# Optimization experiments

Hardware: AMD Instinct MI355X
Metric: run time of the kernel (lower is better)

Reference implementation:

```python
import jax, jax.numpy as jnp
import numpy as np


def _lstm(x, W, U, b, return_sequences):
    # x: [B,T,F]; W: [F,4H]; U: [H,4H]; b: [4H]. Keras gate order: i,f,c,o.
    B = x.shape[0]
    H = U.shape[0]
    # precompute input projection for all timesteps: [T,B,4H]
    xW = jnp.einsum('btf,fg->tbg', x, W) + b
    h0 = jnp.zeros((B, H), x.dtype)
    c0 = jnp.zeros((B, H), x.dtype)

    def step(carry, xw):
        h, c = carry
        z = xw + h @ U  # [B,4H]
        i, f, g, o = jnp.split(z, 4, axis=-1)
        i = jax.nn.sigmoid(i)
        f = jax.nn.sigmoid(f)
        g = jax.nn.relu(g)      # activation='relu' on candidate
        o = jax.nn.sigmoid(o)
        c = f * c + i * g
        h = o * jax.nn.relu(c)  # activation='relu' on cell output
        return (h, c), h

    (hT, _), hs = jax.lax.scan(step, (h0, c0), xW)
    if return_sequences:
        return jnp.transpose(hs, (1, 0, 2))  # [B,T,H]
    return hT  # [B,H]


def setup_inputs() -> dict:
    key = jax.random.key(0)
    ks = jax.random.split(key, 11)
    B, T, F = 512, 512, 64
    H1, H2, D1, D2 = 128, 64, 25, 1
    s = 0.05  # small weight scale keeps the relu-LSTM recurrence numerically stable
    return {
        'x':   jax.random.normal(ks[0], (B, T, F), jnp.float32),
        'W1':  jax.random.normal(ks[1], (F, 4 * H1), jnp.float32) * s,
        'U1':  jax.random.normal(ks[2], (H1, 4 * H1), jnp.float32) * s,
        'b1':  jnp.zeros((4 * H1,), jnp.float32),
        'W2':  jax.random.normal(ks[3], (H1, 4 * H2), jnp.float32) * s,
        'U2':  jax.random.normal(ks[4], (H2, 4 * H2), jnp.float32) * s,
        'b2':  jnp.zeros((4 * H2,), jnp.float32),
        'Wd1': jax.random.normal(ks[5], (H2, D1), jnp.float32) * s,
        'bd1': jnp.zeros((D1,), jnp.float32),
        'Wd2': jax.random.normal(ks[6], (D1, D2), jnp.float32) * s,
        'bd2': jnp.zeros((D2,), jnp.float32),
    }


def reference(x, W1, U1, b1, W2, U2, b2, Wd1, bd1, Wd2, bd2):
    h = _lstm(x, W1, U1, b1, return_sequences=True)   # [B,T,128]
    h = _lstm(h, W2, U2, b2, return_sequences=False)  # [B,64]
    h = h @ Wd1 + bd1                                  # [B,25]
    return h @ Wd2 + bd2                               # [B,1]
```

## Files before the change

kernel.cpp:

```cpp
#include <hip/hip_runtime.h>
#include <type_traits>

typedef _Float16 f16;
typedef _Float16 f16x4 __attribute__((ext_vector_type(4)));
typedef _Float16 f16x8 __attribute__((ext_vector_type(8)));
typedef float    f32x4 __attribute__((ext_vector_type(4)));

constexpr int TT = 512;
constexpr int FF = 64;
constexpr int H1 = 128;
constexpr int H2 = 64;
constexpr int D1 = 25;
constexpr int S1 = 136;
constexpr int S2 = 72;
constexpr int XC = 8;
constexpr float L2E = 1.44269504088896f;

__device__ __forceinline__ float sigm2(float z) {
    return __builtin_amdgcn_rcpf(1.f + __builtin_amdgcn_exp2f(-z));
}

__device__ __forceinline__ f32x4 mfma16(f16x8 a, f16x8 b, f32x4 c) {
    return __builtin_amdgcn_mfma_f32_16x16x32_f16(a, b, c, 0, 0, 0);
}

__device__ __forceinline__ void gl_lds16(const f16* g, f16* l) {
    __builtin_amdgcn_global_load_lds(
        (const __attribute__((address_space(1))) unsigned int*)g,
        (__attribute__((address_space(3))) unsigned int*)l, 16, 0, 0);
}

__global__ void cvt_x_kernel(const float* __restrict__ x, f16* __restrict__ xh) {
    const size_t i = ((size_t)blockIdx.x * blockDim.x + threadIdx.x) * 4;
    const float4 v = *(const float4*)(x + i);
    f16x4 h; h[0] = (f16)v.x; h[1] = (f16)v.y; h[2] = (f16)v.z; h[3] = (f16)v.w;
    *(f16x4*)(xh + i) = h;
}

__global__ __launch_bounds__(768, 3)
void lstm_pipe12(const f16* __restrict__ xh, const float* __restrict__ W1,
                 const float* __restrict__ U1, const float* __restrict__ b1,
                 const float* __restrict__ W2, const float* __restrict__ U2,
                 const float* __restrict__ b2, const float* __restrict__ Wd1,
                 const float* __restrict__ bd1,const float* __restrict__ Wd2,
                 const float* __restrict__ bd2, float* __restrict__ out)
{
    const int tid  = threadIdx.x;
    const int w    = tid >> 6;
    const int lane = tid & 63;
    const int quad = lane >> 4;
    const int lid  = lane & 15;
    const int b0   = blockIdx.x * 16;
    const bool isL1 = (w < 8);
    const int  j    = isL1 ? w : (w - 8);

    __shared__ __align__(16) f16 h1b[2][16][S1];
    __shared__ __align__(16) f16 h2b[2][16][S2];
    __shared__ __align__(16) f16 xlds[2][XC * 8 * 16 * 8];
    __shared__ float h2f[16][H2];
    __shared__ float dsh[16][D1];

    for (int i = tid; i < 2 * 16 * S1 / 2; i += 768) ((unsigned*)h1b)[i] = 0u;
    for (int i = tid; i < 2 * 16 * S2 / 2; i += 768) ((unsigned*)h2b)[i] = 0u;

    for (int s = tid; s < XC * 8 * 16; s += 768) {
        const int tl = s >> 7, fs = (s >> 4) & 7, row = s & 15;
        const f16* gp = xh + ((size_t)(b0 + row) * TT + tl) * FF + fs * 8;
        gl_lds16(gp, &xlds[0][(s >> 6) * 512]);
    }

    f16x8 wt[4][6];
    f32x4 bsp[4];
    float cs[4] = {0.f, 0.f, 0.f, 0.f};

    if (isL1) {
#pragma unroll
        for (int g = 0; g < 4; ++g) {
            const float sc = (g == 2) ? 1.f : L2E;
            const int n = 128 * g + 16 * w + lid;
#pragma unroll
            for (int rr = 0; rr < 4; ++rr)
                bsp[g][rr] = b1[128 * g + 16 * w + quad * 4 + rr] * sc;
#pragma unroll
            for (int c = 0; c < 4; ++c) {
                f16x8 f;
#pragma unroll
                for (int e = 0; e < 8; ++e)
                    f[e] = (f16)(U1[(32 * c + quad * 8 + e) * 512 + n] * sc);
                wt[g][c] = f;
            }
#pragma unroll
            for (int c = 0; c < 2; ++c) {
                f16x8 f;
#pragma unroll
                for (int e = 0; e < 8; ++e)
                    f[e] = (f16)(W1[(32 * c + quad * 8 + e) * 512 + n] * sc);
                wt[g][4 + c] = f;
            }
        }
    } else {
#pragma unroll
        for (int g = 0; g < 4; ++g) {
            const float sc = (g == 2) ? 1.f : L2E;
            const int n = 64 * g + 16 * j + lid;
#pragma unroll
            for (int rr = 0; rr < 4; ++rr)
                bsp[g][rr] = b2[64 * g + 16 * j + quad * 4 + rr] * sc;
#pragma unroll
            for (int c = 0; c < 4; ++c) {
                f16x8 f;
#pragma unroll
                for (int e = 0; e < 8; ++e)
                    f[e] = (f16)(W2[(32 * c + quad * 8 + e) * 256 + n] * sc);
                wt[g][c] = f;
            }
#pragma unroll
            for (int c = 0; c < 2; ++c) {
                f16x8 f;
#pragma unroll
                for (int e = 0; e < 8; ++e)
                    f[e] = (f16)(U2[(32 * c + quad * 8 + e) * 256 + n] * sc);
                wt[g][4 + c] = f;
            }
        }
    }
    __syncthreads();

    if (isL1) asm volatile("s_setprio 1");

    auto step = [&](auto parc, int i) {
        constexpr int PAR = decltype(parc)::value;
        constexpr int PR = PAR ^ 1;
        constexpr int PW = PAR;
        constexpr int QR = PAR;
        constexpr int QW = PAR ^ 1;
        if (isL1) {
            const f16* xc = &xlds[(i >> 3) & 1][(i & 7) * 1024];
            f16x8 fr0 = *(const f16x8*)&h1b[PR][lid][quad * 8];
            f16x8 fr1 = *(const f16x8*)&h1b[PR][lid][32 + quad * 8];
            f16x8 fr2 = *(const f16x8*)&h1b[PR][lid][64 + quad * 8];
            f16x8 fr3 = *(const f16x8*)&h1b[PR][lid][96 + quad * 8];
            f16x8 xf0 = *(const f16x8*)&xc[(quad * 16 + lid) * 8];
            f16x8 xf1 = *(const f16x8*)&xc[((4 + quad) * 16 + lid) * 8];
            f32x4 acc[4];
#pragma unroll
            for (int g = 0; g < 4; ++g) {
                f32x4 a = mfma16(wt[g][0], fr0, bsp[g]);
                a = mfma16(wt[g][1], fr1, a);
                a = mfma16(wt[g][2], fr2, a);
                a = mfma16(wt[g][3], fr3, a);
                a = mfma16(wt[g][4], xf0, a);
                a = mfma16(wt[g][5], xf1, a);
                acc[g] = a;
            }
            f16x4 hp;
#pragma unroll
            for (int r = 0; r < 4; ++r) {
                const float ig = sigm2(acc[0][r]);
                const float fg = sigm2(acc[1][r]);
                const float gg = fmaxf(acc[2][r], 0.f);
                const float og = sigm2(acc[3][r]);
                const float cc = fg * cs[r] + ig * gg;
                cs[r] = cc;
                hp[r] = (f16)(og * fmaxf(cc, 0.f));
            }
            *(f16x4*)&h1b[PW][lid][16 * w + quad * 4] = hp;
        } else {
            if (i >= 1) {
                f16x8 fr0 = *(const f16x8*)&h1b[PR][lid][quad * 8];
                f16x8 fr1 = *(const f16x8*)&h1b[PR][lid][32 + quad * 8];
                f16x8 fr2 = *(const f16x8*)&h1b[PR][lid][64 + quad * 8];
                f16x8 fr3 = *(const f16x8*)&h1b[PR][lid][96 + quad * 8];
                f16x8 fr4 = *(const f16x8*)&h2b[QR][lid][quad * 8];
                f16x8 fr5 = *(const f16x8*)&h2b[QR][lid][32 + quad * 8];
                f32x4 acc[4];
#pragma unroll
                for (int g = 0; g < 4; ++g) {
                    f32x4 a = mfma16(wt[g][0], fr0, bsp[g]);
                    a = mfma16(wt[g][1], fr1, a);
                    a = mfma16(wt[g][2], fr2, a);
                    a = mfma16(wt[g][3], fr3, a);
                    a = mfma16(wt[g][4], fr4, a);
                    a = mfma16(wt[g][5], fr5, a);
                    acc[g] = a;
                }
                f16x4 hp;
#pragma unroll
                for (int r = 0; r < 4; ++r) {
                    const float ig = sigm2(acc[0][r]);
                    const float fg = sigm2(acc[1][r]);
                    const float gg = fmaxf(acc[2][r], 0.f);
                    const float og = sigm2(acc[3][r]);
                    const float cc = fg * cs[r] + ig * gg;
                    cs[r] = cc;
                    hp[r] = (f16)(og * fmaxf(cc, 0.f));
                }
                *(f16x4*)&h2b[QW][lid][16 * j + quad * 4] = hp;
            }
        }
    };

    for (int ii = 0; ii < TT; ii += 2) {
        if ((ii & (XC - 1)) == 0 && ii + XC < TT) {
            const int nc = (ii >> 3) + 1;
            f16* dst = xlds[nc & 1];
            for (int s = tid; s < XC * 8 * 16; s += 768) {
                const int tl = s >> 7, fs = (s >> 4) & 7, row = s & 15;
                const f16* gp = xh + ((size_t)(b0 + row) * TT + (nc * XC + tl)) * FF + fs * 8;
                gl_lds16(gp, &dst[(s >> 6) * 512]);
            }
        }
        step(std::integral_constant<int, 0>{}, ii);
        __syncthreads();
        step(std::integral_constant<int, 1>{}, ii + 1);
        __syncthreads();
    }

    if (isL1) asm volatile("s_setprio 0");

    if (!isL1) {
        f16x8 fr0 = *(const f16x8*)&h1b[1][lid][quad * 8];
        f16x8 fr1 = *(const f16x8*)&h1b[1][lid][32 + quad * 8];
        f16x8 fr2 = *(const f16x8*)&h1b[1][lid][64 + quad * 8];
        f16x8 fr3 = *(const f16x8*)&h1b[1][lid][96 + quad * 8];
        f16x8 fr4 = *(const f16x8*)&h2b[0][lid][quad * 8];
        f16x8 fr5 = *(const f16x8*)&h2b[0][lid][32 + quad * 8];
        f32x4 acc[4];
#pragma unroll
        for (int g = 0; g < 4; ++g) {
            f32x4 a = mfma16(wt[g][0], fr0, bsp[g]);
            a = mfma16(wt[g][1], fr1, a);
            a = mfma16(wt[g][2], fr2, a);
            a = mfma16(wt[g][3], fr3, a);
            a = mfma16(wt[g][4], fr4, a);
            a = mfma16(wt[g][5], fr5, a);
            acc[g] = a;
        }
        float4 ho;
#pragma unroll
        for (int r = 0; r < 4; ++r) {
            const float ig = sigm2(acc[0][r]);
            const float fg = sigm2(acc[1][r]);
            const float gg = fmaxf(acc[2][r], 0.f);
            const float og = sigm2(acc[3][r]);
            const float cc = fg * cs[r] + ig * gg;
            (&ho.x)[r] = og * fmaxf(cc, 0.f);
        }
        *(float4*)&h2f[lid][16 * j + quad * 4] = ho;
    }
    __syncthreads();

    for (int idx = tid; idx < 16 * D1; idx += 768) {
        const int bq = idx / D1, p = idx % D1;
        float d = bd1[p];
#pragma unroll
        for (int k = 0; k < H2; ++k) d += h2f[bq][k] * Wd1[k * D1 + p];
        dsh[bq][p] = d * Wd2[p];
    }
    __syncthreads();
    if (tid < 16) {
        float o = bd2[0];
#pragma unroll
        for (int p = 0; p < D1; ++p) o += dsh[tid][p];
        out[b0 + tid] = o;
    }
}

extern "C" void kernel_launch(void* const* d_in, const int* in_sizes, int n_in,
                              void* d_out, int out_size, void* d_ws, size_t ws_size,
                              hipStream_t stream) {
    (void)in_sizes; (void)n_in; (void)out_size; (void)ws_size;
    const float* x   = (const float*)d_in[0];
    const float* W1  = (const float*)d_in[1];
    const float* U1  = (const float*)d_in[2];
    const float* b1  = (const float*)d_in[3];
    const float* W2  = (const float*)d_in[4];
    const float* U2  = (const float*)d_in[5];
    const float* b2  = (const float*)d_in[6];
    const float* Wd1 = (const float*)d_in[7];
    const float* bd1 = (const float*)d_in[8];
    const float* Wd2 = (const float*)d_in[9];
    const float* bd2 = (const float*)d_in[10];
    float* out = (float*)d_out;
    f16*   xh  = (f16*)d_ws;

    const int nx = 512 * 512 * 64;
    cvt_x_kernel<<<dim3(nx / (256 * 4)), dim3(256), 0, stream>>>(x, xh);
    lstm_pipe12<<<dim3(32), dim3(768), 0, stream>>>(
        xh, W1, U1, b1, W2, U2, b2, Wd1, bd1, Wd2, bd2, out);
}
```

Baseline: 680.7 us.

## Precompute layer-1 input projection in a parallel kernel before the recurrence

A new parallel kernel computes x@W1+b1 for all timesteps with MFMA and stores it as fp16 in the workspace (256 MB). The recurrent kernel then streams these precomputed gate inputs as the accumulator seed, so layer-1 waves drop the input-projection MFMAs from the serial critical path. In exchange it adds a large global write and read of the projected tensor and depends on workspace size, falling back to the old path otherwise.

```diff
diff --git a/kernel.cpp b/kernel.cpp
--- a/kernel.cpp
+++ b/kernel.cpp
@@ -29,6 +29,282 @@
         (const __attribute__((address_space(1))) unsigned int*)g,
         (__attribute__((address_space(3))) unsigned int*)l, 16, 0, 0);
 }
+
+
+__global__ __launch_bounds__(512)
+void prep_xw(const float* __restrict__ x, const float* __restrict__ W1,
+             const float* __restrict__ b1, f16* __restrict__ xw)
+{
+    __shared__ __align__(16) f16 wlds[512][72];
+    __shared__ __align__(16) float blds[512];
+    const int tid = threadIdx.x;
+
+    for (int idx = tid; idx < 64 * 512; idx += 512) {
+        const int k = idx >> 9, col = idx & 511;
+        const float sc = ((col >> 7) == 2) ? 1.f : L2E;
+        wlds[col][k] = (f16)(W1[idx] * sc);
+    }
+    blds[tid] = b1[tid] * (((tid >> 7) == 2) ? 1.f : L2E);
+    __syncthreads();
+
+    const int wv = tid >> 6, lane = tid & 63, quad = lane >> 4, lid = lane & 15;
+    const int row = blockIdx.x * 128 + wv * 16 + lid;
+
+    f16x8 xf[2];
+#pragma unroll
+    for (int c = 0; c < 2; ++c) {
+        const float4 v0 = *(const float4*)(x + (size_t)row * FF + 32 * c + quad * 8);
+        const float4 v1 = *(const float4*)(x + (size_t)row * FF + 32 * c + quad * 8 + 4);
+        f16x8 f;
+        f[0] = (f16)v0.x; f[1] = (f16)v0.y; f[2] = (f16)v0.z; f[3] = (f16)v0.w;
+        f[4] = (f16)v1.x; f[5] = (f16)v1.y; f[6] = (f16)v1.z; f[7] = (f16)v1.w;
+        xf[c] = f;
+    }
+
+#pragma unroll 4
+    for (int cg = 0; cg < 32; ++cg) {
+        const f16* wp = &wlds[16 * cg + lid][0];
+        const f16x8 a0 = *(const f16x8*)(wp + quad * 8);
+        const f16x8 a1 = *(const f16x8*)(wp + 32 + quad * 8);
+        const f32x4 bv = *(const f32x4*)&blds[16 * cg + quad * 4];
+        f32x4 acc = mfma16(a0, xf[0], bv);
+        acc = mfma16(a1, xf[1], acc);
+        f16x4 o;
+#pragma unroll
+        for (int r = 0; r < 4; ++r) o[r] = (f16)acc[r];
+        *(f16x4*)&xw[(size_t)row * 512 + 16 * cg + quad * 4] = o;
+    }
+}
+
+__global__ __launch_bounds__(768, 3)
+void lstm_pipe12_xw(const f16* __restrict__ xw, const float* __restrict__ U1,
+                    const float* __restrict__ W2, const float* __restrict__ U2,
+                    const float* __restrict__ b2, const float* __restrict__ Wd1,
+                    const float* __restrict__ bd1,const float* __restrict__ Wd2,
+                    const float* __restrict__ bd2, float* __restrict__ out)
+{
+    const int tid  = threadIdx.x;
+    const int w    = tid >> 6;
+    const int lane = tid & 63;
+    const int quad = lane >> 4;
+    const int lid  = lane & 15;
+    const int b0   = blockIdx.x * 16;
+    const bool isL1 = (w < 8);
+    const int  j    = isL1 ? w : (w - 8);
+
+    __shared__ __align__(16) f16 h1b[2][16][S1];
+    __shared__ __align__(16) f16 h2b[2][16][S2];
+    __shared__ float h2f[16][H2];
+    __shared__ float dsh[16][D1];
+
+    for (int i = tid; i < 2 * 16 * S1 / 2; i += 768) ((unsigned*)h1b)[i] = 0u;
+    for (int i = tid; i < 2 * 16 * S2 / 2; i += 768) ((unsigned*)h2b)[i] = 0u;
+
+    f16x8 wt[4][6];
+    f32x4 bsp[4];
+    float cs[4] = {0.f, 0.f, 0.f, 0.f};
+
+    if (isL1) {
+#pragma unroll
+        for (int g = 0; g < 4; ++g) {
+            const float sc = (g == 2) ? 1.f : L2E;
+            const int n = 128 * g + 16 * w + lid;
+#pragma unroll
+            for (int c = 0; c < 4; ++c) {
+                f16x8 f;
+#pragma unroll
+                for (int e = 0; e < 8; ++e)
+                    f[e] = (f16)(U1[(32 * c + quad * 8 + e) * 512 + n] * sc);
+                wt[g][c] = f;
+            }
+        }
+    } else {
+#pragma unroll
+        for (int g = 0; g < 4; ++g) {
+            const float sc = (g == 2) ? 1.f : L2E;
+            const int n = 64 * g + 16 * j + lid;
+#pragma unroll
+            for (int rr = 0; rr < 4; ++rr)
+                bsp[g][rr] = b2[64 * g + 16 * j + quad * 4 + rr] * sc;
+#pragma unroll
+            for (int c = 0; c < 4; ++c) {
+                f16x8 f;
+#pragma unroll
+                for (int e = 0; e < 8; ++e)
+                    f[e] = (f16)(W2[(32 * c + quad * 8 + e) * 256 + n] * sc);
+                wt[g][c] = f;
+            }
+#pragma unroll
+            for (int c = 0; c < 2; ++c) {
+                f16x8 f;
+#pragma unroll
+                for (int e = 0; e < 8; ++e)
+                    f[e] = (f16)(U2[(32 * c + quad * 8 + e) * 256 + n] * sc);
+                wt[g][4 + c] = f;
+            }
+        }
+    }
+
+    const f16* pxw = nullptr;
+    if (isL1) pxw = xw + (size_t)(b0 + lid) * TT * 512 + 16 * w + quad * 4;
+
+    f16x4 xa[2][4], xb[2][4];
+    if (isL1) {
+#pragma unroll
+        for (int g = 0; g < 4; ++g) {
+            xa[0][g] = *(const f16x4*)(pxw + (size_t)0 * 512 + 128 * g);
+            xa[1][g] = *(const f16x4*)(pxw + (size_t)1 * 512 + 128 * g);
+        }
+    }
+    __syncthreads();
+
+    if (isL1) asm volatile("s_setprio 1");
+
+    auto step = [&](auto parc, int i, const f16x4 (&xv)[4]) {
+        constexpr int PAR = decltype(parc)::value;
+        constexpr int PR = PAR ^ 1;
+        constexpr int PW = PAR;
+        constexpr int QR = PAR;
+        constexpr int QW = PAR ^ 1;
+        if (isL1) {
+            f16x8 fr0 = *(const f16x8*)&h1b[PR][lid][quad * 8];
+            f16x8 fr1 = *(const f16x8*)&h1b[PR][lid][32 + quad * 8];
+            f16x8 fr2 = *(const f16x8*)&h1b[PR][lid][64 + quad * 8];
+            f16x8 fr3 = *(const f16x8*)&h1b[PR][lid][96 + quad * 8];
+            f32x4 acc[4];
+#pragma unroll
+            for (int g = 0; g < 4; ++g) {
+                f32x4 ci;
+#pragma unroll
+                for (int r = 0; r < 4; ++r) ci[r] = (float)xv[g][r];
+                f32x4 a = mfma16(wt[g][0], fr0, ci);
+                a = mfma16(wt[g][1], fr1, a);
+                a = mfma16(wt[g][2], fr2, a);
+                a = mfma16(wt[g][3], fr3, a);
+                acc[g] = a;
+            }
+            f16x4 hp;
+#pragma unroll
+            for (int r = 0; r < 4; ++r) {
+                const float ig = sigm2(acc[0][r]);
+                const float fg = sigm2(acc[1][r]);
+                const float gg = fmaxf(acc[2][r], 0.f);
+                const float og = sigm2(acc[3][r]);
+                const float cc = fg * cs[r] + ig * gg;
+                cs[r] = cc;
+                hp[r] = (f16)(og * fmaxf(cc, 0.f));
+            }
+            *(f16x4*)&h1b[PW][lid][16 * w + quad * 4] = hp;
+        } else {
+            if (i >= 1) {
+                f16x8 fr0 = *(const f16x8*)&h1b[PR][lid][quad * 8];
+                f16x8 fr1 = *(const f16x8*)&h1b[PR][lid][32 + quad * 8];
+                f16x8 fr2 = *(const f16x8*)&h1b[PR][lid][64 + quad * 8];
+                f16x8 fr3 = *(const f16x8*)&h1b[PR][lid][96 + quad * 8];
+                f16x8 fr4 = *(const f16x8*)&h2b[QR][lid][quad * 8];
+                f16x8 fr5 = *(const f16x8*)&h2b[QR][lid][32 + quad * 8];
+                f32x4 acc[4];
+#pragma unroll
+                for (int g = 0; g < 4; ++g) {
+                    f32x4 a = mfma16(wt[g][0], fr0, bsp[g]);
+                    a = mfma16(wt[g][1], fr1, a);
+                    a = mfma16(wt[g][2], fr2, a);
+                    a = mfma16(wt[g][3], fr3, a);
+                    a = mfma16(wt[g][4], fr4, a);
+                    a = mfma16(wt[g][5], fr5, a);
+                    acc[g] = a;
+                }
+                f16x4 hp;
+#pragma unroll
+                for (int r = 0; r < 4; ++r) {
+                    const float ig = sigm2(acc[0][r]);
+                    const float fg = sigm2(acc[1][r]);
+                    const float gg = fmaxf(acc[2][r], 0.f);
+                    const float og = sigm2(acc[3][r]);
+                    const float cc = fg * cs[r] + ig * gg;
+                    cs[r] = cc;
+                    hp[r] = (f16)(og * fmaxf(cc, 0.f));
+                }
+                *(f16x4*)&h2b[QW][lid][16 * j + quad * 4] = hp;
+            }
+        }
+    };
+
+    for (int ii = 0; ii < TT; ii += 4) {
+        if (isL1) {
+#pragma unroll
+            for (int g = 0; g < 4; ++g) {
+                xb[0][g] = *(const f16x4*)(pxw + (size_t)(ii + 2) * 512 + 128 * g);
+                xb[1][g] = *(const f16x4*)(pxw + (size_t)(ii + 3) * 512 + 128 * g);
+            }
+        }
+        step(std::integral_constant<int, 0>{}, ii, xa[0]);
+        __syncthreads();
+        step(std::integral_constant<int, 1>{}, ii + 1, xa[1]);
+        __syncthreads();
+        if (isL1 && ii + 4 < TT) {
+#pragma unroll
+            for (int g = 0; g < 4; ++g) {
+                xa[0][g] = *(const f16x4*)(pxw + (size_t)(ii + 4) * 512 + 128 * g);
+                xa[1][g] = *(const f16x4*)(pxw + (size_t)(ii + 5) * 512 + 128 * g);
+            }
+        }
+        step(std::integral_constant<int, 0>{}, ii + 2, xb[0]);
+        __syncthreads();
+        step(std::integral_constant<int, 1>{}, ii + 3, xb[1]);
+        __syncthreads();
+    }
+
+    if (isL1) asm volatile("s_setprio 0");
+
+    if (!isL1) {
+        f16x8 fr0 = *(const f16x8*)&h1b[1][lid][quad * 8];
+        f16x8 fr1 = *(const f16x8*)&h1b[1][lid][32 + quad * 8];
+        f16x8 fr2 = *(const f16x8*)&h1b[1][lid][64 + quad * 8];
+        f16x8 fr3 = *(const f16x8*)&h1b[1][lid][96 + quad * 8];
+        f16x8 fr4 = *(const f16x8*)&h2b[0][lid][quad * 8];
+        f16x8 fr5 = *(const f16x8*)&h2b[0][lid][32 + quad * 8];
+        f32x4 acc[4];
+#pragma unroll
+        for (int g = 0; g < 4; ++g) {
+            f32x4 a = mfma16(wt[g][0], fr0, bsp[g]);
+            a = mfma16(wt[g][1], fr1, a);
+            a = mfma16(wt[g][2], fr2, a);
+            a = mfma16(wt[g][3], fr3, a);
+            a = mfma16(wt[g][4], fr4, a);
+            a = mfma16(wt[g][5], fr5, a);
+            acc[g] = a;
+        }
+        float4 ho;
+#pragma unroll
+        for (int r = 0; r < 4; ++r) {
+            const float ig = sigm2(acc[0][r]);
+            const float fg = sigm2(acc[1][r]);
+            const float gg = fmaxf(acc[2][r], 0.f);
+            const float og = sigm2(acc[3][r]);
+            const float cc = fg * cs[r] + ig * gg;
+            (&ho.x)[r] = og * fmaxf(cc, 0.f);
+        }
+        *(float4*)&h2f[lid][16 * j + quad * 4] = ho;
+    }
+    __syncthreads();
+
+    for (int idx = tid; idx < 16 * D1; idx += 768) {
+        const int bq = idx / D1, p = idx % D1;
+        float d = bd1[p];
+#pragma unroll
+        for (int k = 0; k < H2; ++k) d += h2f[bq][k] * Wd1[k * D1 + p];
+        dsh[bq][p] = d * Wd2[p];
+    }
+    __syncthreads();
+    if (tid < 16) {
+        float o = bd2[0];
+#pragma unroll
+        for (int p = 0; p < D1; ++p) o += dsh[tid][p];
+        out[b0 + tid] = o;
+    }
+}
+
 
 __global__ void cvt_x_kernel(const float* __restrict__ x, f16* __restrict__ xh) {
     const size_t i = ((size_t)blockIdx.x * blockDim.x + threadIdx.x) * 4;
@@ -269,7 +545,7 @@
 extern "C" void kernel_launch(void* const* d_in, const int* in_sizes, int n_in,
                               void* d_out, int out_size, void* d_ws, size_t ws_size,
                               hipStream_t stream) {
-    (void)in_sizes; (void)n_in; (void)out_size; (void)ws_size;
+    (void)in_sizes; (void)n_in; (void)out_size;
     const float* x   = (const float*)d_in[0];
     const float* W1  = (const float*)d_in[1];
     const float* U1  = (const float*)d_in[2];
@@ -282,10 +558,19 @@
     const float* Wd2 = (const float*)d_in[9];
     const float* bd2 = (const float*)d_in[10];
     float* out = (float*)d_out;
-    f16*   xh  = (f16*)d_ws;
-
-    const int nx = 512 * 512 * 64;
-    cvt_x_kernel<<<dim3(nx / (256 * 4)), dim3(256), 0, stream>>>(x, xh);
-    lstm_pipe12<<<dim3(32), dim3(768), 0, stream>>>(
-        xh, W1, U1, b1, W2, U2, b2, Wd1, bd1, Wd2, bd2, out);
-}
+
+    constexpr size_t XW_BYTES = (size_t)512 * 512 * 512 * sizeof(f16);
+
+    if (ws_size >= XW_BYTES) {
+        f16* xwp = (f16*)d_ws;
+        prep_xw<<<dim3(2048), dim3(512), 0, stream>>>(x, W1, b1, xwp);
+        lstm_pipe12_xw<<<dim3(32), dim3(768), 0, stream>>>(
+            xwp, U1, W2, U2, b2, Wd1, bd1, Wd2, bd2, out);
+    } else {
+        f16* xh = (f16*)d_ws;
+        const int nx = 512 * 512 * 64;
+        cvt_x_kernel<<<dim3(nx / (256 * 4)), dim3(256), 0, stream>>>(x, xh);
+        lstm_pipe12<<<dim3(32), dim3(768), 0, stream>>>(
+            xh, W1, U1, b1, W2, U2, b2, Wd1, bd1, Wd2, bd2, out);
+    }
+}
```

Result: slower. 1.483 ms (+117.9%).

## Consolidate LSTM layers into four waves each handling two L1 tiles and one L2 tile

Applied to the files above, without the earlier changes.

Shrinks the block from twelve waves (eight layer-1, four layer-2) to four waves, each computing two layer-1 gate column tiles and one layer-2 tile per step. The h and x fragments are loaded once per wave and reused across all three tiles, and the wave-priority hints are dropped. This aims to cut barrier cost and redundant LDS fragment loads, but triples the per-wave MFMA chain and register-resident weights, which risks longer serial latency and register spills.

```diff
diff --git a/kernel.cpp b/kernel.cpp
--- a/kernel.cpp
+++ b/kernel.cpp
@@ -37,13 +37,13 @@
     *(f16x4*)(xh + i) = h;
 }
 
-__global__ __launch_bounds__(768, 3)
-void lstm_pipe12(const f16* __restrict__ xh, const float* __restrict__ W1,
-                 const float* __restrict__ U1, const float* __restrict__ b1,
-                 const float* __restrict__ W2, const float* __restrict__ U2,
-                 const float* __restrict__ b2, const float* __restrict__ Wd1,
-                 const float* __restrict__ bd1,const float* __restrict__ Wd2,
-                 const float* __restrict__ bd2, float* __restrict__ out)
+__global__ __launch_bounds__(256, 1)
+void lstm_q4(const f16* __restrict__ xh, const float* __restrict__ W1,
+             const float* __restrict__ U1, const float* __restrict__ b1,
+             const float* __restrict__ W2, const float* __restrict__ U2,
+             const float* __restrict__ b2, const float* __restrict__ Wd1,
+             const float* __restrict__ bd1,const float* __restrict__ Wd2,
+             const float* __restrict__ bd2, float* __restrict__ out)
 {
     const int tid  = threadIdx.x;
     const int w    = tid >> 6;
@@ -51,8 +51,6 @@
     const int quad = lane >> 4;
     const int lid  = lane & 15;
     const int b0   = blockIdx.x * 16;
-    const bool isL1 = (w < 8);
-    const int  j    = isL1 ? w : (w - 8);
 
     __shared__ __align__(16) f16 h1b[2][16][S1];
     __shared__ __align__(16) f16 h2b[2][16][S2];
@@ -60,34 +58,37 @@
     __shared__ float h2f[16][H2];
     __shared__ float dsh[16][D1];
 
-    for (int i = tid; i < 2 * 16 * S1 / 2; i += 768) ((unsigned*)h1b)[i] = 0u;
-    for (int i = tid; i < 2 * 16 * S2 / 2; i += 768) ((unsigned*)h2b)[i] = 0u;
-
-    for (int s = tid; s < XC * 8 * 16; s += 768) {
+    for (int i = tid; i < 2 * 16 * S1 / 2; i += 256) ((unsigned*)h1b)[i] = 0u;
+    for (int i = tid; i < 2 * 16 * S2 / 2; i += 256) ((unsigned*)h2b)[i] = 0u;
+
+    for (int s = tid; s < XC * 8 * 16; s += 256) {
         const int tl = s >> 7, fs = (s >> 4) & 7, row = s & 15;
         const f16* gp = xh + ((size_t)(b0 + row) * TT + tl) * FF + fs * 8;
         gl_lds16(gp, &xlds[0][(s >> 6) * 512]);
     }
 
-    f16x8 wt[4][6];
-    f32x4 bsp[4];
-    float cs[4] = {0.f, 0.f, 0.f, 0.f};
-
-    if (isL1) {
+    f16x8 wtA[4][6], wtB[4][6], wtC[4][6];
+    f32x4 bspA[4], bspB[4], bspC[4];
+    float csA[4] = {0.f, 0.f, 0.f, 0.f};
+    float csB[4] = {0.f, 0.f, 0.f, 0.f};
+    float csC[4] = {0.f, 0.f, 0.f, 0.f};
+
+    {
+        const int cg = 2 * w;
 #pragma unroll
         for (int g = 0; g < 4; ++g) {
             const float sc = (g == 2) ? 1.f : L2E;
-            const int n = 128 * g + 16 * w + lid;
+            const int n = 128 * g + 16 * cg + lid;
 #pragma unroll
             for (int rr = 0; rr < 4; ++rr)
-                bsp[g][rr] = b1[128 * g + 16 * w + quad * 4 + rr] * sc;
+                bspA[g][rr] = b1[128 * g + 16 * cg + quad * 4 + rr] * sc;
 #pragma unroll
             for (int c = 0; c < 4; ++c) {
                 f16x8 f;
 #pragma unroll
                 for (int e = 0; e < 8; ++e)
                     f[e] = (f16)(U1[(32 * c + quad * 8 + e) * 512 + n] * sc);
-                wt[g][c] = f;
+                wtA[g][c] = f;
             }
 #pragma unroll
             for (int c = 0; c < 2; ++c) {
@@ -95,24 +96,52 @@
 #pragma unroll
                 for (int e = 0; e < 8; ++e)
                     f[e] = (f16)(W1[(32 * c + quad * 8 + e) * 512 + n] * sc);
-                wt[g][4 + c] = f;
-            }
-        }
-    } else {
+                wtA[g][4 + c] = f;
+            }
+        }
+    }
+    {
+        const int cg = 2 * w + 1;
 #pragma unroll
         for (int g = 0; g < 4; ++g) {
             const float sc = (g == 2) ? 1.f : L2E;
-            const int n = 64 * g + 16 * j + lid;
+            const int n = 128 * g + 16 * cg + lid;
 #pragma unroll
             for (int rr = 0; rr < 4; ++rr)
-                bsp[g][rr] = b2[64 * g + 16 * j + quad * 4 + rr] * sc;
+                bspB[g][rr] = b1[128 * g + 16 * cg + quad * 4 + rr] * sc;
 #pragma unroll
             for (int c = 0; c < 4; ++c) {
                 f16x8 f;
 #pragma unroll
                 for (int e = 0; e < 8; ++e)
+                    f[e] = (f16)(U1[(32 * c + quad * 8 + e) * 512 + n] * sc);
+                wtB[g][c] = f;
+            }
+#pragma unroll
+            for (int c = 0; c < 2; ++c) {
+                f16x8 f;
+#pragma unroll
+                for (int e = 0; e < 8; ++e)
+                    f[e] = (f16)(W1[(32 * c + quad * 8 + e) * 512 + n] * sc);
+                wtB[g][4 + c] = f;
+            }
+        }
+    }
+    {
+#pragma unroll
+        for (int g = 0; g < 4; ++g) {
+            const float sc = (g == 2) ? 1.f : L2E;
+            const int n = 64 * g + 16 * w + lid;
+#pragma unroll
+            for (int rr = 0; rr < 4; ++rr)
+                bspC[g][rr] = b2[64 * g + 16 * w + quad * 4 + rr] * sc;
+#pragma unroll
+            for (int c = 0; c < 4; ++c) {
+                f16x8 f;
+#pragma unroll
+                for (int e = 0; e < 8; ++e)
                     f[e] = (f16)(W2[(32 * c + quad * 8 + e) * 256 + n] * sc);
-                wt[g][c] = f;
+                wtC[g][c] = f;
             }
 #pragma unroll
             for (int c = 0; c < 2; ++c) {
@@ -120,13 +149,11 @@
 #pragma unroll
                 for (int e = 0; e < 8; ++e)
                     f[e] = (f16)(U2[(32 * c + quad * 8 + e) * 256 + n] * sc);
-                wt[g][4 + c] = f;
+                wtC[g][4 + c] = f;
             }
         }
     }
     __syncthreads();
-
-    if (isL1) asm volatile("s_setprio 1");
 
     auto step = [&](auto parc, int i) {
         constexpr int PAR = decltype(parc)::value;
@@ -134,69 +161,105 @@
         constexpr int PW = PAR;
         constexpr int QR = PAR;
         constexpr int QW = PAR ^ 1;
-        if (isL1) {
-            const f16* xc = &xlds[(i >> 3) & 1][(i & 7) * 1024];
-            f16x8 fr0 = *(const f16x8*)&h1b[PR][lid][quad * 8];
-            f16x8 fr1 = *(const f16x8*)&h1b[PR][lid][32 + quad * 8];
-            f16x8 fr2 = *(const f16x8*)&h1b[PR][lid][64 + quad * 8];
-            f16x8 fr3 = *(const f16x8*)&h1b[PR][lid][96 + quad * 8];
-            f16x8 xf0 = *(const f16x8*)&xc[(quad * 16 + lid) * 8];
-            f16x8 xf1 = *(const f16x8*)&xc[((4 + quad) * 16 + lid) * 8];
-            f32x4 acc[4];
+        const f16* xc = &xlds[(i >> 3) & 1][(i & 7) * 1024];
+        f16x8 xf0 = *(const f16x8*)&xc[(quad * 16 + lid) * 8];
+        f16x8 xf1 = *(const f16x8*)&xc[((4 + quad) * 16 + lid) * 8];
+        f16x8 fr0 = *(const f16x8*)&h1b[PR][lid][quad * 8];
+        f16x8 fr1 = *(const f16x8*)&h1b[PR][lid][32 + quad * 8];
+        f16x8 fr2 = *(const f16x8*)&h1b[PR][lid][64 + quad * 8];
+        f16x8 fr3 = *(const f16x8*)&h1b[PR][lid][96 + quad * 8];
+        f16x8 fr4 = *(const f16x8*)&h2b[QR][lid][quad * 8];
+        f16x8 fr5 = *(const f16x8*)&h2b[QR][lid][32 + quad * 8];
+
+        f32x4 accA[4];
+#pragma unroll
+        for (int g = 0; g < 4; ++g) {
+            f32x4 a = mfma16(wtA[g][0], fr0, bspA[g]);
+            a = mfma16(wtA[g][1], fr1, a);
+            a = mfma16(wtA[g][2], fr2, a);
+            a = mfma16(wtA[g][3], fr3, a);
+            a = mfma16(wtA[g][4], xf0, a);
+            a = mfma16(wtA[g][5], xf1, a);
+            accA[g] = a;
+        }
+        f32x4 accB[4];
+#pragma unroll
+        for (int g = 0; g < 4; ++g) {
+            f32x4 a = mfma16(wtB[g][0], fr0, bspB[g]);
+            a = mfma16(wtB[g][1], fr1, a);
+            a = mfma16(wtB[g][2], fr2, a);
+            a = mfma16(wtB[g][3], fr3, a);
+            a = mfma16(wtB[g][4], xf0, a);
+            a = mfma16(wtB[g][5], xf1, a);
+            accB[g] = a;
+        }
+        {
+            f16x4 hp;
+#pragma unroll
+            for (int r = 0; r < 4; ++r) {
+                const float ig = sigm2(accA[0][r]);
+                const float fg = sigm2(accA[1][r]);
+                const float gg = fmaxf(accA[2][r], 0.f);
+                const float og = sigm2(accA[3][r]);
+                const float cc = fg * csA[r] + ig * gg;
+                csA[r] = cc;
+                hp[r] = (f16)(og * fmaxf(cc, 0.f));
+            }
+            *(f16x4*)&h1b[PW][lid][16 * (2 * w) + quad * 4] = hp;
+        }
+        if (i >= 1) {
+            f32x4 accC[4];
 #pragma unroll
             for (int g = 0; g < 4; ++g) {
-                f32x4 a = mfma16(wt[g][0], fr0, bsp[g]);
-                a = mfma16(wt[g][1], fr1, a);
-                a = mfma16(wt[g][2], fr2, a);
-                a = mfma16(wt[g][3], fr3, a);
-                a = mfma16(wt[g][4], xf0, a);
-                a = mfma16(wt[g][5], xf1, a);
-                acc[g] = a;
-            }
-            f16x4 hp;
-#pragma unroll
-            for (int r = 0; r < 4; ++r) {
-                const float ig = sigm2(acc[0][r]);
-                const float fg = sigm2(acc[1][r]);
-                const float gg = fmaxf(acc[2][r], 0.f);
-                const float og = sigm2(acc[3][r]);
-                const float cc = fg * cs[r] + ig * gg;
-                cs[r] = cc;
-                hp[r] = (f16)(og * fmaxf(cc, 0.f));
-            }
-            *(f16x4*)&h1b[PW][lid][16 * w + quad * 4] = hp;
-        } else {
-            if (i >= 1) {
-                f16x8 fr0 = *(const f16x8*)&h1b[PR][lid][quad * 8];
-                f16x8 fr1 = *(const f16x8*)&h1b[PR][lid][32 + quad * 8];
-                f16x8 fr2 = *(const f16x8*)&h1b[PR][lid][64 + quad * 8];
-                f16x8 fr3 = *(const f16x8*)&h1b[PR][lid][96 + quad * 8];
-                f16x8 fr4 = *(const f16x8*)&h2b[QR][lid][quad * 8];
-                f16x8 fr5 = *(const f16x8*)&h2b[QR][lid][32 + quad * 8];
-                f32x4 acc[4];
-#pragma unroll
-                for (int g = 0; g < 4; ++g) {
-                    f32x4 a = mfma16(wt[g][0], fr0, bsp[g]);
-                    a = mfma16(wt[g][1], fr1, a);
-                    a = mfma16(wt[g][2], fr2, a);
-                    a = mfma16(wt[g][3], fr3, a);
-                    a = mfma16(wt[g][4], fr4, a);
-                    a = mfma16(wt[g][5], fr5, a);
-                    acc[g] = a;
-                }
+                f32x4 a = mfma16(wtC[g][0], fr0, bspC[g]);
+                a = mfma16(wtC[g][1], fr1, a);
+                a = mfma16(wtC[g][2], fr2, a);
+                a = mfma16(wtC[g][3], fr3, a);
+                a = mfma16(wtC[g][4], fr4, a);
+                a = mfma16(wtC[g][5], fr5, a);
+                accC[g] = a;
+            }
+            {
                 f16x4 hp;
 #pragma unroll
                 for (int r = 0; r < 4; ++r) {
-                    const float ig = sigm2(acc[0][r]);
-                    const float fg = sigm2(acc[1][r]);
-                    const float gg = fmaxf(acc[2][r], 0.f);
-                    const float og = sigm2(acc[3][r]);
-                    const float cc = fg * cs[r] + ig * gg;
-                    cs[r] = cc;
+                    const float ig = sigm2(accB[0][r]);
+                    const float fg = sigm2(accB[1][r]);
+                    const float gg = fmaxf(accB[2][r], 0.f);
+                    const float og = sigm2(accB[3][r]);
+                    const float cc = fg * csB[r] + ig * gg;
+                    csB[r] = cc;
                     hp[r] = (f16)(og * fmaxf(cc, 0.f));
                 }
-                *(f16x4*)&h2b[QW][lid][16 * j + quad * 4] = hp;
-            }
+                *(f16x4*)&h1b[PW][lid][16 * (2 * w + 1) + quad * 4] = hp;
+            }
+            {
+                f16x4 hp;
+#pragma unroll
+                for (int r = 0; r < 4; ++r) {
+                    const float ig = sigm2(accC[0][r]);
+                    const float fg = sigm2(accC[1][r]);
+                    const float gg = fmaxf(accC[2][r], 0.f);
+                    const float og = sigm2(accC[3][r]);
+                    const float cc = fg * csC[r] + ig * gg;
+                    csC[r] = cc;
+                    hp[r] = (f16)(og * fmaxf(cc, 0.f));
+                }
+                *(f16x4*)&h2b[QW][lid][16 * w + quad * 4] = hp;
+            }
+        } else {
+            f16x4 hp;
+#pragma unroll
+            for (int r = 0; r < 4; ++r) {
+                const float ig = sigm2(accB[0][r]);
+                const float fg = sigm2(accB[1][r]);
+                const float gg = fmaxf(accB[2][r], 0.f);
+                const float og = sigm2(accB[3][r]);
+                const float cc = fg * csB[r] + ig * gg;
+                csB[r] = cc;
+                hp[r] = (f16)(og * fmaxf(cc, 0.f));
+            }
+            *(f16x4*)&h1b[PW][lid][16 * (2 * w + 1) + quad * 4] = hp;
         }
     };
 
@@ -204,7 +267,7 @@
         if ((ii & (XC - 1)) == 0 && ii + XC < TT) {
             const int nc = (ii >> 3) + 1;
             f16* dst = xlds[nc & 1];
-            for (int s = tid; s < XC * 8 * 16; s += 768) {
+            for (int s = tid; s < XC * 8 * 16; s += 256) {
                 const int tl = s >> 7, fs = (s >> 4) & 7, row = s & 15;
                 const f16* gp = xh + ((size_t)(b0 + row) * TT + (nc * XC + tl)) * FF + fs * 8;
                 gl_lds16(gp, &dst[(s >> 6) * 512]);
@@ -216,9 +279,7 @@
         __syncthreads();
     }
 
-    if (isL1) asm volatile("s_setprio 0");
-
-    if (!isL1) {
+    {
         f16x8 fr0 = *(const f16x8*)&h1b[1][lid][quad * 8];
         f16x8 fr1 = *(const f16x8*)&h1b[1][lid][32 + quad * 8];
         f16x8 fr2 = *(const f16x8*)&h1b[1][lid][64 + quad * 8];
@@ -228,12 +289,12 @@
         f32x4 acc[4];
 #pragma unroll
         for (int g = 0; g < 4; ++g) {
-            f32x4 a = mfma16(wt[g][0], fr0, bsp[g]);
-            a = mfma16(wt[g][1], fr1, a);
-            a = mfma16(wt[g][2], fr2, a);
-            a = mfma16(wt[g][3], fr3, a);
-            a = mfma16(wt[g][4], fr4, a);
-            a = mfma16(wt[g][5], fr5, a);
+            f32x4 a = mfma16(wtC[g][0], fr0, bspC[g]);
+            a = mfma16(wtC[g][1], fr1, a);
+            a = mfma16(wtC[g][2], fr2, a);
+            a = mfma16(wtC[g][3], fr3, a);
+            a = mfma16(wtC[g][4], fr4, a);
+            a = mfma16(wtC[g][5], fr5, a);
             acc[g] = a;
         }
         float4 ho;
@@ -243,14 +304,14 @@
             const float fg = sigm2(acc[1][r]);
             const float gg = fmaxf(acc[2][r], 0.f);
             const float og = sigm2(acc[3][r]);
-            const float cc = fg * cs[r] + ig * gg;
+            const float cc = fg * csC[r] + ig * gg;
             (&ho.x)[r] = og * fmaxf(cc, 0.f);
         }
-        *(float4*)&h2f[lid][16 * j + quad * 4] = ho;
+        *(float4*)&h2f[lid][16 * w + quad * 4] = ho;
     }
     __syncthreads();
 
-    for (int idx = tid; idx < 16 * D1; idx += 768) {
+    for (int idx = tid; idx < 16 * D1; idx += 256) {
         const int bq = idx / D1, p = idx % D1;
         float d = bd1[p];
 #pragma unroll
@@ -286,6 +347,6 @@
 
     const int nx = 512 * 512 * 64;
     cvt_x_kernel<<<dim3(nx / (256 * 4)), dim3(256), 0, stream>>>(x, xh);
-    lstm_pipe12<<<dim3(32), dim3(768), 0, stream>>>(
+    lstm_q4<<<dim3(32), dim3(256), 0, stream>>>(
         xh, W1, U1, b1, W2, U2, b2, Wd1, bd1, Wd2, bd2, out);
 }
```

Result: slower. 879.3 us (+29.2%).
